# Performance work log

Measured on AMD Instinct MI355X. Metric: run time of the kernel, lower is better.

## Reference

```python
import jax, jax.numpy as jnp
import numpy as np
import math

IN_FEATURES = 4096
OUT_FEATURES = 4096
N_ROWS = 8192
EPS = 1e-6
ROOT2 = math.sqrt(2.0)


def setup_inputs() -> dict:
    key = jax.random.key(0)
    k1, k2 = jax.random.split(key)
    # p_x: probabilities in [0,1]
    p_x = jax.random.uniform(k1, (N_ROWS, IN_FEATURES), dtype=jnp.float32)
    # weight ~ Uniform(-2, 2) per reset_parameters
    weight = jax.random.uniform(k2, (OUT_FEATURES, IN_FEATURES), dtype=jnp.float32, minval=-2.0, maxval=2.0)
    return {"p_x": p_x, "weight": weight}


def reference(p_x, weight):
    in_features = weight.shape[1]
    threshold = -(-in_features // 2)  # ceil(in_features / 2)
    p_w = jax.nn.sigmoid(weight)  # (O, I)
    # p_success = 2*p_w*p_x + 1 - p_x - p_w = c*p_x + d, with:
    c = 2.0 * p_w - 1.0          # (O, I)
    d = 1.0 - p_w                # (O, I)
    # mu = sum_i p_success = p_x @ c^T + sum_i d   -- never materialize (..., O, I)
    mu = jnp.einsum('ni,oi->no', p_x, c) + jnp.sum(d, axis=-1)  # (N, O)
    # sum_i p_success^2 = p_x^2 @ (c^2)^T + 2 * p_x @ (c*d)^T + sum_i d^2
    sum_sq = (jnp.einsum('ni,oi->no', p_x * p_x, c * c)
              + 2.0 * jnp.einsum('ni,oi->no', p_x, c * d)
              + jnp.sum(d * d, axis=-1))  # (N, O)
    # sum p_success*(1 - p_success) = mu - sum_sq
    sigma = jnp.sqrt(mu - sum_sq + EPS)  # (N, O)
    p_actives = 0.5 - 0.5 * jax.lax.erf((threshold - 0.5 - mu) / (sigma * ROOT2))
    return p_actives
```

## Files before the change

kernel.cpp:

```cpp
#include <hip/hip_runtime.h>
#include <hip/hip_bf16.h>
#include <math.h>
#include <cstdint>

#define KDIM 4096
#define ODIM 4096
#define MDIM 8192
#define EPSF 1e-6f
#define TM05 2047.5f

typedef __bf16 bf16x8 __attribute__((ext_vector_type(8)));
typedef float f32x4 __attribute__((ext_vector_type(4)));
typedef unsigned short u16;

#define XY_DELTA (MDIM * KDIM)
#define CD_DELTA (ODIM * KDIM)

#define NITER (KDIM / 128)

__device__ __forceinline__ u16 f2bf(float f) {
  __hip_bfloat16 h = __float2bfloat16(f);
  return __builtin_bit_cast(u16, h);
}
__device__ __forceinline__ float bf2f(u16 b) {
  unsigned int u = ((unsigned int)b) << 16;
  return __builtin_bit_cast(float, u);
}

__device__ __forceinline__ void async_cp16(void* lds, const void* g) {
  __builtin_amdgcn_global_load_lds(
      (__attribute__((address_space(1))) void*)(uintptr_t)g,
      (__attribute__((address_space(3))) void*)lds, 16, 0, 0);
}

__global__ void prep_x_kernel(const float4* __restrict__ x4,
                              ushort4* __restrict__ Xb,
                              ushort4* __restrict__ Yb) {
  int i = blockIdx.x * blockDim.x + threadIdx.x;
  float4 v = x4[i];
  ushort4 xo, yo;
  xo.x = f2bf(v.x); xo.y = f2bf(v.y); xo.z = f2bf(v.z); xo.w = f2bf(v.w);
  yo.x = f2bf(v.x * (1.0f - v.x));
  yo.y = f2bf(v.y * (1.0f - v.y));
  yo.z = f2bf(v.z * (1.0f - v.z));
  yo.w = f2bf(v.w * (1.0f - v.w));
  Xb[i] = xo;
  Yb[i] = yo;
}

__device__ __forceinline__ void wcomp(float w, u16& cb, u16& c2b, float& sd, float& sde) {
  float pw = 1.0f / (1.0f + __expf(-w));
  float c  = 2.0f * pw - 1.0f;
  float d  = 1.0f - pw;
  cb  = f2bf(c);
  c2b = f2bf(c * c);
  sd  += d;
  sde += d * pw;
}

__global__ void prep_w_kernel(const float4* __restrict__ w4,
                              ushort4* __restrict__ Cb,
                              ushort4* __restrict__ C2b,
                              float* __restrict__ sumd,
                              float* __restrict__ sumde) {
  const int o = blockIdx.x;
  const int t = threadIdx.x;
  const float4* wr = w4 + (size_t)o * (KDIM / 4);
  ushort4* cr  = Cb  + (size_t)o * (KDIM / 4);
  ushort4* c2r = C2b + (size_t)o * (KDIM / 4);
  float sd = 0.f, sde = 0.f;
#pragma unroll
  for (int it = 0; it < KDIM / 4 / 256; ++it) {
    int k4 = t + it * 256;
    float4 w = wr[k4];
    ushort4 co, c2o;
    wcomp(w.x, co.x, c2o.x, sd, sde);
    wcomp(w.y, co.y, c2o.y, sd, sde);
    wcomp(w.z, co.z, c2o.z, sd, sde);
    wcomp(w.w, co.w, c2o.w, sd, sde);
    cr[k4]  = co;
    c2r[k4] = c2o;
  }
#pragma unroll
  for (int off = 32; off > 0; off >>= 1) {
    sd  += __shfl_down(sd, off);
    sde += __shfl_down(sde, off);
  }
  __shared__ float red[8];
  if ((t & 63) == 0) { red[t >> 6] = sd; red[4 + (t >> 6)] = sde; }
  __syncthreads();
  if (t == 0) {
    sumd[o]  = red[0] + red[1] + red[2] + red[3];
    sumde[o] = red[4] + red[5] + red[6] + red[7];
  }
}


#define STG_H(bb, isB, half, srcB, tt) do {                                    \
    char* _d = smem + (bb) * 65536 + (isB) * 32768 + (half) * 16384 + tid * 16;\
    const u16* _s = (srcB) + (size_t)((half) * 128) * KDIM + (size_t)(tt) * 64;\
    async_cp16(_d, _s);                                                        \
    async_cp16(_d + 8192, _s + (size_t)64 * KDIM);                             \
  } while (0)

#define PHASE(bb, p, STG, VM) {                                                \
    const char* Ab = smem + (bb) * 65536;                                      \
    const char* Bb = Ab + 32768;                                               \
    bf16x8 a0k0 = *(const bf16x8*)(Ab + arow + ((p) * 2 + 0) * 2048 + g0);     \
    bf16x8 a0k1 = *(const bf16x8*)(Ab + arow + ((p) * 2 + 0) * 2048 + g1);     \
    bf16x8 a1k0 = *(const bf16x8*)(Ab + arow + ((p) * 2 + 1) * 2048 + g0);     \
    bf16x8 a1k1 = *(const bf16x8*)(Ab + arow + ((p) * 2 + 1) * 2048 + g1);     \
    if ((p) == 0) {                                                            \
      _Pragma("unroll") for (int j = 0; j < 4; ++j) {                          \
        b0[j] = *(const bf16x8*)(Bb + brow + j * 2048 + g0);                   \
        b1[j] = *(const bf16x8*)(Bb + brow + j * 2048 + g1);                   \
      }                                                                        \
    }                                                                          \
    STG;                                                                       \
    __builtin_amdgcn_s_barrier();                                              \
    asm volatile("s_waitcnt lgkmcnt(0)" ::: "memory");                         \
    __builtin_amdgcn_sched_barrier(0);                                         \
    __builtin_amdgcn_s_setprio(1);                                             \
    _Pragma("unroll") for (int j = 0; j < 4; ++j)                              \
      acc[(p)*2+0][j] = __builtin_amdgcn_mfma_f32_16x16x32_bf16(a0k0, b0[j], acc[(p)*2+0][j], 0, 0, 0); \
    _Pragma("unroll") for (int j = 0; j < 4; ++j)                              \
      acc[(p)*2+1][j] = __builtin_amdgcn_mfma_f32_16x16x32_bf16(a1k0, b0[j], acc[(p)*2+1][j], 0, 0, 0); \
    _Pragma("unroll") for (int j = 0; j < 4; ++j)                              \
      acc[(p)*2+0][j] = __builtin_amdgcn_mfma_f32_16x16x32_bf16(a0k1, b1[j], acc[(p)*2+0][j], 0, 0, 0); \
    _Pragma("unroll") for (int j = 0; j < 4; ++j)                              \
      acc[(p)*2+1][j] = __builtin_amdgcn_mfma_f32_16x16x32_bf16(a1k1, b1[j], acc[(p)*2+1][j], 0, 0, 0); \
    __builtin_amdgcn_s_setprio(0);                                             \
    VM;                                                                        \
    __builtin_amdgcn_s_barrier();                                              \
  }

template <int PASS>
__global__ __launch_bounds__(512, 2) void gemm_pass_kernel(
    const u16* __restrict__ Ag, const u16* __restrict__ Bg,
    const float* __restrict__ sumd, const float* __restrict__ sumde,
    float* __restrict__ out) {
  __shared__ __attribute__((aligned(128))) char smem[2 * 65536];

  const int tid  = threadIdx.x;
  const int lane = tid & 63;
  const int wave = tid >> 6;
  const int wr   = wave >> 2;
  const int wc   = wave & 3;
  const int quad = lane >> 4;
  const int r16  = lane & 15;

  const int raw = blockIdx.x;
  const int wg  = (raw & 7) * 64 + (raw >> 3);
  const int n0  = (wg >> 5) * 256;
  const int m0  = (wg & 31) * 256;

  const int srow = tid >> 3;
  const int scol = ((tid & 7) ^ (srow & 7)) * 8;
  const u16* gA = Ag + (size_t)(m0 + srow) * KDIM + scol;
  const u16* gB = Bg + (size_t)(n0 + srow) * KDIM + scol;

  const int r7   = r16 & 7;
  const int g0   = (quad ^ r7) * 16;
  const int g1   = ((4 | quad) ^ r7) * 16;
  const int arow = (wr * 128 + r16) * 128;
  const int brow = (wc * 64 + r16) * 128;

  f32x4 acc[8][4];
#pragma unroll
  for (int i = 0; i < 8; ++i)
#pragma unroll
    for (int j = 0; j < 4; ++j) acc[i][j] = f32x4{0.f, 0.f, 0.f, 0.f};

  bf16x8 b0[4], b1[4];

  STG_H(0, 0, 0, gA, 0); STG_H(0, 0, 1, gA, 0);
  STG_H(0, 1, 0, gB, 0); STG_H(0, 1, 1, gB, 0);
  STG_H(1, 1, 0, gB, 1); STG_H(1, 1, 1, gB, 1);
  asm volatile("s_waitcnt vmcnt(4)" ::: "memory");
  __builtin_amdgcn_s_barrier();

  for (int s = 0; s < NITER; ++s) {
    const bool nlast = (s + 1 < NITER);
    const int t1 = 2 * s + 1, t2 = 2 * s + 2, t3 = 2 * s + 3;

    PHASE(0, 0, STG_H(1, 0, 0, gA, t1), )
    PHASE(0, 1, STG_H(1, 0, 1, gA, t1), )
    PHASE(0, 2, if (nlast) STG_H(0, 1, 0, gB, t2), )
    PHASE(0, 3, if (nlast) STG_H(0, 1, 1, gB, t2),
          if (nlast) { asm volatile("s_waitcnt vmcnt(4)" ::: "memory"); }
          else       { asm volatile("s_waitcnt vmcnt(0)" ::: "memory"); })
    PHASE(1, 0, if (nlast) STG_H(0, 0, 0, gA, t2), )
    PHASE(1, 1, if (nlast) STG_H(0, 0, 1, gA, t2), )
    PHASE(1, 2, if (nlast) STG_H(1, 1, 0, gB, t3), )
    PHASE(1, 3, if (nlast) STG_H(1, 1, 1, gB, t3),
          if (nlast) { asm volatile("s_waitcnt vmcnt(4)" ::: "memory"); }
          else       { asm volatile("s_waitcnt vmcnt(0)" ::: "memory"); })
  }

  if (PASS == 0) {
#pragma unroll
    for (int j = 0; j < 4; ++j) {
      const int col = n0 + wc * 64 + j * 16 + r16;
#pragma unroll
      for (int i = 0; i < 8; ++i) {
        const int row = m0 + wr * 128 + i * 16 + quad * 4;
        f32x4 v = acc[i][j];
#pragma unroll
        for (int r = 0; r < 4; ++r) out[(size_t)(row + r) * ODIM + col] = v[r];
      }
    }
  } else {
    const float inv_rt2 = 0.70710678118654752f;
#pragma unroll
    for (int j = 0; j < 4; ++j) {
      const int col = n0 + wc * 64 + j * 16 + r16;
      const float sd  = sumd[col];
      const float sde = sumde[col] + EPSF;
#pragma unroll
      for (int i = 0; i < 8; ++i) {
        const int row = m0 + wr * 128 + i * 16 + quad * 4;
        f32x4 m4 = acc[i][j];
#pragma unroll
        for (int r = 0; r < 4; ++r) {
          float var = out[(size_t)(row + r) * ODIM + col] + sde;
          float mu  = m4[r] + sd;
          float z = (TM05 - mu) * rsqrtf(var) * inv_rt2;
          out[(size_t)(row + r) * ODIM + col] = 0.5f * erfcf(z);
        }
      }
    }
  }
}

extern "C" void kernel_launch(void* const* d_in, const int* in_sizes, int n_in,
                              void* d_out, int out_size, void* d_ws, size_t ws_size,
                              hipStream_t stream) {
  const float* p_x    = (const float*)d_in[0];
  const float* weight = (const float*)d_in[1];
  float* out = (float*)d_out;
  char* ws = (char*)d_ws;

  u16* Cb      = (u16*)(ws);
  u16* C2b     = (u16*)(ws + 33554432);
  float* sumd  = (float*)(ws + 67108864);
  float* sumde = (float*)(ws + 67125248);
  u16* Xb      = (u16*)(ws + 67141632);
  u16* Yb      = (u16*)(ws + 134250496);

  prep_w_kernel<<<ODIM, 256, 0, stream>>>((const float4*)weight, (ushort4*)Cb,
                                          (ushort4*)C2b, sumd, sumde);
  prep_x_kernel<<<(MDIM * KDIM / 4) / 256, 256, 0, stream>>>((const float4*)p_x,
                                                             (ushort4*)Xb,
                                                             (ushort4*)Yb);
  const int nwg = (MDIM / 256) * (ODIM / 256);
  gemm_pass_kernel<0><<<nwg, 512, 0, stream>>>(Yb, C2b, sumd, sumde, out);
  gemm_pass_kernel<1><<<nwg, 512, 0, stream>>>(Xb, Cb, sumd, sumde, out);
}
```

Measured before the change: 774.3 us.

## Restructure GEMM phases to one barrier per phase and k-half ordering

Reorders the inner MFMA phases so each phase processes one k-half (g0 or g1) across four A row tiles, reusing B fragments loaded once per k-half, instead of two A tiles across both k-halves. It removes one of the two s_barriers per phase, fusing the vmcnt wait with the barrier in inline asm. It also replaces the per-iteration tile index math with incrementing global pointers. The aim is to cut barrier overhead and address arithmetic, at the risk of weaker LDS/compute overlap or a race from the removed barrier.

```diff
diff --git a/kernel.cpp b/kernel.cpp
--- a/kernel.cpp
+++ b/kernel.cpp
@@ -96,42 +96,42 @@
 }
 
 
-#define STG_H(bb, isB, half, srcB, tt) do {                                    \
+#define STG2(bb, isB, half, src, koff) do {                                    \
     char* _d = smem + (bb) * 65536 + (isB) * 32768 + (half) * 16384 + tid * 16;\
-    const u16* _s = (srcB) + (size_t)((half) * 128) * KDIM + (size_t)(tt) * 64;\
+    const u16* _s = (src) + (size_t)((half) * 128) * KDIM + (koff);            \
     async_cp16(_d, _s);                                                        \
     async_cp16(_d + 8192, _s + (size_t)64 * KDIM);                             \
   } while (0)
 
-#define PHASE(bb, p, STG, VM) {                                                \
+#define BAR   asm volatile("s_barrier" ::: "memory")
+#define BARV4 asm volatile("s_waitcnt vmcnt(4)\n\ts_barrier" ::: "memory")
+#define BARV0 asm volatile("s_waitcnt vmcnt(0)\n\ts_barrier" ::: "memory")
+
+#define PH(bb, AI, MO, GK, BARR, DOB, STG, ENDBAR) {                           \
     const char* Ab = smem + (bb) * 65536;                                      \
     const char* Bb = Ab + 32768;                                               \
-    bf16x8 a0k0 = *(const bf16x8*)(Ab + arow + ((p) * 2 + 0) * 2048 + g0);     \
-    bf16x8 a0k1 = *(const bf16x8*)(Ab + arow + ((p) * 2 + 0) * 2048 + g1);     \
-    bf16x8 a1k0 = *(const bf16x8*)(Ab + arow + ((p) * 2 + 1) * 2048 + g0);     \
-    bf16x8 a1k1 = *(const bf16x8*)(Ab + arow + ((p) * 2 + 1) * 2048 + g1);     \
-    if ((p) == 0) {                                                            \
-      _Pragma("unroll") for (int j = 0; j < 4; ++j) {                          \
-        b0[j] = *(const bf16x8*)(Bb + brow + j * 2048 + g0);                   \
-        b1[j] = *(const bf16x8*)(Bb + brow + j * 2048 + g1);                   \
-      }                                                                        \
+    bf16x8 x0 = *(const bf16x8*)(Ab + arow + (MO) + 0 * 2048 + (GK));          \
+    bf16x8 x1 = *(const bf16x8*)(Ab + arow + (MO) + 1 * 2048 + (GK));          \
+    bf16x8 x2 = *(const bf16x8*)(Ab + arow + (MO) + 2 * 2048 + (GK));          \
+    bf16x8 x3 = *(const bf16x8*)(Ab + arow + (MO) + 3 * 2048 + (GK));          \
+    if (DOB) {                                                                 \
+      _Pragma("unroll") for (int j = 0; j < 4; ++j)                            \
+        BARR[j] = *(const bf16x8*)(Bb + brow + j * 2048 + (GK));               \
     }                                                                          \
     STG;                                                                       \
-    __builtin_amdgcn_s_barrier();                                              \
     asm volatile("s_waitcnt lgkmcnt(0)" ::: "memory");                         \
     __builtin_amdgcn_sched_barrier(0);                                         \
     __builtin_amdgcn_s_setprio(1);                                             \
     _Pragma("unroll") for (int j = 0; j < 4; ++j)                              \
-      acc[(p)*2+0][j] = __builtin_amdgcn_mfma_f32_16x16x32_bf16(a0k0, b0[j], acc[(p)*2+0][j], 0, 0, 0); \
-    _Pragma("unroll") for (int j = 0; j < 4; ++j)                              \
-      acc[(p)*2+1][j] = __builtin_amdgcn_mfma_f32_16x16x32_bf16(a1k0, b0[j], acc[(p)*2+1][j], 0, 0, 0); \
-    _Pragma("unroll") for (int j = 0; j < 4; ++j)                              \
-      acc[(p)*2+0][j] = __builtin_amdgcn_mfma_f32_16x16x32_bf16(a0k1, b1[j], acc[(p)*2+0][j], 0, 0, 0); \
-    _Pragma("unroll") for (int j = 0; j < 4; ++j)                              \
-      acc[(p)*2+1][j] = __builtin_amdgcn_mfma_f32_16x16x32_bf16(a1k1, b1[j], acc[(p)*2+1][j], 0, 0, 0); \
+      acc[(AI) + 0][j] = __builtin_amdgcn_mfma_f32_16x16x32_bf16(x0, BARR[j], acc[(AI) + 0][j], 0, 0, 0); \
+    _Pragma("unroll") for (int j = 0; j < 4; ++j)                              \
+      acc[(AI) + 1][j] = __builtin_amdgcn_mfma_f32_16x16x32_bf16(x1, BARR[j], acc[(AI) + 1][j], 0, 0, 0); \
+    _Pragma("unroll") for (int j = 0; j < 4; ++j)                              \
+      acc[(AI) + 2][j] = __builtin_amdgcn_mfma_f32_16x16x32_bf16(x2, BARR[j], acc[(AI) + 2][j], 0, 0, 0); \
+    _Pragma("unroll") for (int j = 0; j < 4; ++j)                              \
+      acc[(AI) + 3][j] = __builtin_amdgcn_mfma_f32_16x16x32_bf16(x3, BARR[j], acc[(AI) + 3][j], 0, 0, 0); \
     __builtin_amdgcn_s_setprio(0);                                             \
-    VM;                                                                        \
-    __builtin_amdgcn_s_barrier();                                              \
+    ENDBAR;                                                                    \
   }
 
 template <int PASS>
@@ -173,28 +173,24 @@
 
   bf16x8 b0[4], b1[4];
 
-  STG_H(0, 0, 0, gA, 0); STG_H(0, 0, 1, gA, 0);
-  STG_H(0, 1, 0, gB, 0); STG_H(0, 1, 1, gB, 0);
-  STG_H(1, 1, 0, gB, 1); STG_H(1, 1, 1, gB, 1);
-  asm volatile("s_waitcnt vmcnt(4)" ::: "memory");
-  __builtin_amdgcn_s_barrier();
+  STG2(0, 0, 0, gA, 0); STG2(0, 0, 1, gA, 0);
+  STG2(0, 1, 0, gB, 0); STG2(0, 1, 1, gB, 0);
+  STG2(1, 1, 0, gB, 64); STG2(1, 1, 1, gB, 64);
+  BARV4;
 
   for (int s = 0; s < NITER; ++s) {
-    const bool nlast = (s + 1 < NITER);
-    const int t1 = 2 * s + 1, t2 = 2 * s + 2, t3 = 2 * s + 3;
-
-    PHASE(0, 0, STG_H(1, 0, 0, gA, t1), )
-    PHASE(0, 1, STG_H(1, 0, 1, gA, t1), )
-    PHASE(0, 2, if (nlast) STG_H(0, 1, 0, gB, t2), )
-    PHASE(0, 3, if (nlast) STG_H(0, 1, 1, gB, t2),
-          if (nlast) { asm volatile("s_waitcnt vmcnt(4)" ::: "memory"); }
-          else       { asm volatile("s_waitcnt vmcnt(0)" ::: "memory"); })
-    PHASE(1, 0, if (nlast) STG_H(0, 0, 0, gA, t2), )
-    PHASE(1, 1, if (nlast) STG_H(0, 0, 1, gA, t2), )
-    PHASE(1, 2, if (nlast) STG_H(1, 1, 0, gB, t3), )
-    PHASE(1, 3, if (nlast) STG_H(1, 1, 1, gB, t3),
-          if (nlast) { asm volatile("s_waitcnt vmcnt(4)" ::: "memory"); }
-          else       { asm volatile("s_waitcnt vmcnt(0)" ::: "memory"); })
+    const bool nl = (s + 1 < NITER);
+    PH(0, 0, 0,    g0, b0, 1, STG2(1, 0, 0, gA, 64), BAR)
+    PH(0, 0, 0,    g1, b1, 1, STG2(1, 0, 1, gA, 64), BAR)
+    PH(0, 4, 8192, g0, b0, 0, if (nl) STG2(0, 1, 0, gB, 128), BAR)
+    PH(0, 4, 8192, g1, b1, 0, if (nl) STG2(0, 1, 1, gB, 128),
+       if (nl) { BARV4; } else { BARV0; })
+    PH(1, 0, 0,    g0, b0, 1, if (nl) STG2(0, 0, 0, gA, 128), BAR)
+    PH(1, 0, 0,    g1, b1, 1, if (nl) STG2(0, 0, 1, gA, 128), BAR)
+    PH(1, 4, 8192, g0, b0, 0, if (nl) STG2(1, 1, 0, gB, 192), BAR)
+    PH(1, 4, 8192, g1, b1, 0, if (nl) STG2(1, 1, 1, gB, 192),
+       if (nl) { BARV4; } else { BARV0; })
+    gA += 128; gB += 128;
   }
 
   if (PASS == 0) {
```

After: 775.5 us. No clear change (+0.1%).
